# Kernel tuning notes

Measured on AMD Instinct MI355X. Metric: run time of the kernel, lower is better.

Reference implementation:

```python
import jax, jax.numpy as jnp
import numpy as np

B, S, D = 4, 2048, 1024
H, DK = 16, 64
NUM_BUCKETS = 32
MAX_DISTANCE = 128
EPS = 1e-6


def _relative_position_bucket(q_len, kv_len):
    # causal (bidirectional=False) T5 bucketization
    ctx = jnp.arange(q_len, dtype=jnp.int32)[:, None]
    mem = jnp.arange(kv_len, dtype=jnp.int32)[None, :]
    rp = mem - ctx                       # [q, kv]
    rp = -jnp.minimum(rp, 0)             # nonnegative distances to the past
    max_exact = NUM_BUCKETS // 2
    is_small = rp < max_exact
    rp_safe = jnp.maximum(rp, 1).astype(jnp.float32)
    large = max_exact + (
        jnp.log(rp_safe / max_exact) / np.log(MAX_DISTANCE / max_exact) * (NUM_BUCKETS - max_exact)
    ).astype(jnp.int32)
    large = jnp.minimum(large, NUM_BUCKETS - 1)
    return jnp.where(is_small, rp, large)  # [q, kv] int32 in [0, NUM_BUCKETS)


def setup_inputs() -> dict:
    key = jax.random.key(0)
    k1, k2, k3, k4 = jax.random.split(key, 4)
    hidden_states = jax.random.normal(k1, (B, S, D), dtype=jnp.float32)
    sequence_mask = jnp.ones((B, S), dtype=bool)
    rms_w = jnp.ones((D,), dtype=jnp.float32)
    W_qkv = jax.random.normal(k2, (D, 3 * H * DK), dtype=jnp.float32) * (D ** -0.5)
    W_o = jax.random.normal(k3, (H * DK, D), dtype=jnp.float32) * ((H * DK) ** -0.5)
    rel_bias = jax.random.normal(k4, (NUM_BUCKETS, H), dtype=jnp.float32)
    return {"hidden_states": hidden_states, "sequence_mask": sequence_mask,
            "rms_w": rms_w, "W_qkv": W_qkv, "W_o": W_o, "rel_bias": rel_bias}


def reference(hidden_states, sequence_mask, rms_w, W_qkv, W_o, rel_bias):
    # RMSNorm
    var = jnp.mean(hidden_states * hidden_states, axis=-1, keepdims=True)
    normed = hidden_states * jax.lax.rsqrt(var + EPS) * rms_w

    # QKV projection -> [B, S, 3, H, DK] -> [B, H, S, DK] each
    qkv = (normed @ W_qkv).reshape(B, S, 3, H, DK)
    q = jnp.transpose(qkv[:, :, 0], (0, 2, 1, 3))
    k = jnp.transpose(qkv[:, :, 1], (0, 2, 1, 3))
    v = jnp.transpose(qkv[:, :, 2], (0, 2, 1, 3))

    # relative position bias: gather [S,S,H] -> [1,H,S,S]
    bucket = _relative_position_bucket(S, S)
    pos_bias = jnp.transpose(rel_bias[bucket], (2, 0, 1))[None]

    # scores (note: T5 does NOT scale by 1/sqrt(dk))
    scores = jnp.einsum("bhqd,bhkd->bhqk", q, k) + pos_bias

    # causal mask combined with sequence mask (True = attend)
    causal = jnp.tril(jnp.ones((S, S), dtype=bool))
    mask = causal[None, None] & sequence_mask[:, None, None, :]
    scores = jnp.where(mask, scores, jnp.finfo(scores.dtype).min)

    attn = jax.nn.softmax(scores.astype(jnp.float32), axis=-1).astype(scores.dtype)
    # dropout p=0 / eval mode -> identity
    ctx = jnp.einsum("bhqk,bhkd->bhqd", attn, v)          # [B,H,S,DK]
    ctx = jnp.transpose(ctx, (0, 2, 1, 3)).reshape(B, S, H * DK)
    out = hidden_states + ctx @ W_o                        # residual
    return out
```

## Files before the change

kernel.cpp:

```cpp
#include <hip/hip_runtime.h>
#include <math.h>


typedef unsigned short ushort_t;
typedef __attribute__((ext_vector_type(8))) short bfrag;
typedef __attribute__((ext_vector_type(4))) float ffrag;

#define MFMA16(a, b, c) __builtin_amdgcn_mfma_f32_16x16x32_bf16((a), (b), (c), 0, 0, 0)
#define LOG2E 1.4426950408889634f

__device__ __forceinline__ void load_lds16(const ushort_t* g, ushort_t* l) {
  __builtin_amdgcn_global_load_lds(
      (const __attribute__((address_space(1))) unsigned int*)g,
      (__attribute__((address_space(3))) unsigned int*)l, 16, 0, 0);
}

__device__ __forceinline__ ushort_t f2bf(float f) {
  union { float f; unsigned u; } x; x.f = f;
  unsigned r = x.u + 0x7FFFu + ((x.u >> 16) & 1u);
  return (ushort_t)(r >> 16);
}
__device__ __forceinline__ float bf2f(ushort_t u) {
  union { unsigned u; float f; } x; x.u = ((unsigned)u) << 16; return x.f;
}
__device__ __forceinline__ unsigned cvtpk(float lo, float hi) {
  unsigned r;
  asm("v_cvt_pk_bf16_f32 %0, %1, %2" : "=v"(r) : "v"(lo), "v"(hi));
  return r;
}
__device__ __forceinline__ float exp2fast(float x) {
  return __builtin_amdgcn_exp2f(x);
}

__global__ __launch_bounds__(256) void norm_cvt_kernel(
    const float* __restrict__ hidden, const float* __restrict__ rms_w,
    ushort_t* __restrict__ normed) {
  const int w = threadIdx.x >> 6, lane = threadIdx.x & 63;
  const int row = blockIdx.x * 4 + w;
  const float* p = hidden + (size_t)row * 1024;
  float4 v[4];
  float s = 0.f;
#pragma unroll
  for (int i = 0; i < 4; ++i) {
    v[i] = *(const float4*)(p + (lane + i * 64) * 4);
    s += v[i].x * v[i].x + v[i].y * v[i].y + v[i].z * v[i].z + v[i].w * v[i].w;
  }
#pragma unroll
  for (int off = 1; off < 64; off <<= 1) s += __shfl_xor(s, off, 64);
  const float scale = rsqrtf(s * (1.0f / 1024.0f) + 1e-6f);
#pragma unroll
  for (int i = 0; i < 4; ++i) {
    const int c0 = (lane + i * 64) * 4;
    float4 wv = *(const float4*)(rms_w + c0);
    ushort4 u;
    u.x = f2bf(v[i].x * scale * wv.x);
    u.y = f2bf(v[i].y * scale * wv.y);
    u.z = f2bf(v[i].z * scale * wv.z);
    u.w = f2bf(v[i].w * scale * wv.w);
    *(ushort4*)(normed + (size_t)row * 1024 + c0) = u;
  }
}

__global__ __launch_bounds__(256) void transpose_cvt_kernel(
    const float* __restrict__ in, ushort_t* __restrict__ out, int R, int C) {
  __shared__ float tile[32][33];
  const int r0 = blockIdx.y * 32, c0 = blockIdx.x * 32;
  const int tr = threadIdx.x >> 5, tc = threadIdx.x & 31;
#pragma unroll
  for (int i = 0; i < 32; i += 8)
    tile[tr + i][tc] = in[(size_t)(r0 + tr + i) * C + c0 + tc];
  __syncthreads();
#pragma unroll
  for (int i = 0; i < 32; i += 8)
    out[(size_t)(c0 + tr + i) * R + r0 + tc] = f2bf(tile[tc][tr + i]);
}

__global__ __launch_bounds__(256) void qkv_mfma_kernel(
    const ushort_t* __restrict__ A, const ushort_t* __restrict__ Bt,
    ushort_t* __restrict__ qbf, ushort_t* __restrict__ kbf,
    ushort_t* __restrict__ vtbf) {
  __shared__ ushort_t At[128 * 32];
  __shared__ ushort_t Bs[128 * 32];
  const int tid = threadIdx.x, w = tid >> 6, lane = tid & 63;
  const int quad = lane >> 4, ln = lane & 15;
  const int wr = w >> 1, wc = w & 1;
  const int id = blockIdx.x;
  const int xcd = id & 7, t = id >> 3;
  const int by = xcd * 8 + t / 24, bx = t % 24;
  const int m0 = by * 128, n0 = bx * 128;
  const int srow = lane >> 2, scol = (lane & 3) * 8;

  ffrag acc[4][4];
#pragma unroll
  for (int i = 0; i < 4; ++i)
#pragma unroll
    for (int j = 0; j < 4; ++j) acc[i][j] = (ffrag)0.f;

  for (int kb = 0; kb < 1024; kb += 32) {
#pragma unroll
    for (int p = 0; p < 2; ++p) {
      load_lds16(A + (size_t)(m0 + (w * 2 + p) * 16 + srow) * 1024 + kb + scol,
                 At + (w * 2 + p) * 512);
      load_lds16(Bt + (size_t)(n0 + (w * 2 + p) * 16 + srow) * 1024 + kb + scol,
                 Bs + (w * 2 + p) * 512);
    }
    __syncthreads();
    bfrag a[4], b[4];
#pragma unroll
    for (int mi = 0; mi < 4; ++mi)
      a[mi] = *(const bfrag*)(At + (wr * 64 + mi * 16 + ln) * 32 + quad * 8);
#pragma unroll
    for (int ni = 0; ni < 4; ++ni)
      b[ni] = *(const bfrag*)(Bs + (wc * 64 + ni * 16 + ln) * 32 + quad * 8);
#pragma unroll
    for (int mi = 0; mi < 4; ++mi)
#pragma unroll
      for (int ni = 0; ni < 4; ++ni)
        acc[mi][ni] = MFMA16(a[mi], b[ni], acc[mi][ni]);
    __syncthreads();
  }

  const int b_idx = m0 >> 11;
  const int cbase = n0 + wc * 64 + ln;
#pragma unroll
  for (int mi = 0; mi < 4; ++mi) {
    const int sbase = (m0 & 2047) + wr * 64 + mi * 16 + quad * 4;
#pragma unroll
    for (int ni = 0; ni < 4; ++ni) {
      const int c = cbase + ni * 16;
      const int three = c >> 10, rem = c & 1023;
      const int h = rem >> 6, dk = rem & 63;
      if (three == 2) {
        ushort4 u;
        u.x = f2bf(acc[mi][ni][0]); u.y = f2bf(acc[mi][ni][1]);
        u.z = f2bf(acc[mi][ni][2]); u.w = f2bf(acc[mi][ni][3]);
        *(ushort4*)(vtbf + ((size_t)(b_idx * 16 + h) * 64 + dk) * 2048 + sbase) = u;
      } else {
        const float sc = (three == 0) ? 1.0f : LOG2E;
        ushort_t* dst = (three == 0 ? qbf : kbf) +
                        ((size_t)(b_idx * 16 + h) * 2048 + sbase) * 64 + dk;
        dst[0]   = f2bf(acc[mi][ni][0] * sc);
        dst[64]  = f2bf(acc[mi][ni][1] * sc);
        dst[128] = f2bf(acc[mi][ni][2] * sc);
        dst[192] = f2bf(acc[mi][ni][3] * sc);
      }
    }
  }
}

__global__ __launch_bounds__(512, 6) void attn_mfma_kernel(
    const ushort_t* __restrict__ qbf, const ushort_t* __restrict__ kbf,
    const ushort_t* __restrict__ vtbf, const float* __restrict__ rel_bias,
    ushort_t* __restrict__ ctx) {
  __shared__ ushort_t Kt[2][2][64][32];
  __shared__ ushort_t Vt[2][2][64][32];
  __shared__ ushort_t Pt[128][64];
  __shared__ ushort_t bias_t[2048];

  const int tid = threadIdx.x, w = tid >> 6, lane = tid & 63;
  const int quad = lane >> 4, ln = lane & 15;
  const int id = blockIdx.x;
  const int bh = id & 63;
  const int qb = 15 - (id >> 6);
  const int h = bh & 15;
  const int nt = 2 * qb + 2;
  const int q0w = qb * 128 + w * 16;

  for (int dist = tid; dist < 2048; dist += 512) {
    int bucket;
    if (dist < 16) bucket = dist;
    else {
      bucket = 16 + (int)(logf((float)dist * (1.0f / 16.0f)) * (16.0f / logf(8.0f)));
      if (bucket > 31) bucket = 31;
    }
    bias_t[dist] = f2bf(rel_bias[bucket * 16 + h] * LOG2E);
  }
  const float c31 = bf2f(f2bf(rel_bias[31 * 16 + h] * LOG2E));
  __syncthreads();

  const size_t khead = (size_t)bh * 2048 * 64;
  const int skf = tid >> 8;
  const int srow = (tid >> 2) & 63;
  const int ssw = ((tid & 3) ^ ((srow >> 1) & 3)) * 8;
  const int rsw = ((ln >> 1) & 3) * 8;
  const int psw = (ln & 7) * 8;

  bfrag aq[2];
#pragma unroll
  for (int kf = 0; kf < 2; ++kf)
    aq[kf] = *(const bfrag*)(qbf + ((size_t)bh * 2048 + q0w + ln) * 64 +
                             kf * 32 + quad * 8);

  bfrag ones;
#pragma unroll
  for (int i = 0; i < 8; ++i) ones[i] = (short)0x3F80;

  ffrag o[4], l_acc;
#pragma unroll
  for (int nd = 0; nd < 4; ++nd) o[nd] = (ffrag)0.f;
  l_acc = (ffrag)0.f;
  float m_run = -3.0e38f;

  load_lds16(kbf + khead + (size_t)srow * 64 + skf * 32 + ssw,
             &Kt[0][0][0][0] + tid * 8);
  load_lds16(vtbf + khead + (size_t)srow * 2048 + 0 + skf * 32 + ssw,
             &Vt[0][0][0][0] + tid * 8);

  int cur = 0;
  for (int j = 0; j < nt; ++j) {
    const int key0 = j * 64;
    asm volatile("s_waitcnt vmcnt(0)" ::: "memory");
    __builtin_amdgcn_s_barrier();

    if (j + 1 < nt) {
      const int nk0 = key0 + 64;
      load_lds16(kbf + khead + (size_t)(nk0 + srow) * 64 + skf * 32 + ssw,
                 &Kt[cur ^ 1][0][0][0] + tid * 8);
      load_lds16(vtbf + khead + (size_t)srow * 2048 + nk0 + skf * 32 + ssw,
                 &Vt[cur ^ 1][0][0][0] + tid * 8);
    }

    if (key0 <= q0w + 15) {
      ffrag s[4];
#pragma unroll
      for (int mi = 0; mi < 4; ++mi) s[mi] = (ffrag)0.f;
      __builtin_amdgcn_s_setprio(1);
#pragma unroll
      for (int kf = 0; kf < 2; ++kf)
#pragma unroll
        for (int mi = 0; mi < 4; ++mi) {
          bfrag ak = *(const bfrag*)&Kt[cur][kf][mi * 16 + ln][(quad * 8) ^ rsw];
          s[mi] = MFMA16(ak, aq[kf], s[mi]);
        }
      __builtin_amdgcn_s_setprio(0);

      const bool diagT = (key0 + 63 > q0w);
      const bool fastT = (key0 + 176 <= q0w);
      float sbias = 0.f;
      if (fastT) {
        sbias = c31;
      } else if (diagT) {
        const int q = q0w + ln;
#pragma unroll
        for (int mi = 0; mi < 4; ++mi) {
          const int keyb = key0 + mi * 16 + quad * 4;
#pragma unroll
          for (int r = 0; r < 4; ++r) {
            const int dist = q - (keyb + r);
            const int db = dist < 0 ? 0 : dist;
            s[mi][r] = (dist < 0) ? -3.0e38f : (s[mi][r] + bf2f(bias_t[db]));
          }
        }
      } else {
        const int q = q0w + ln;
#pragma unroll
        for (int mi = 0; mi < 4; ++mi) {
          const int keyb = key0 + mi * 16 + quad * 4;
#pragma unroll
          for (int r = 0; r < 4; ++r)
            s[mi][r] += bf2f(bias_t[q - (keyb + r)]);
        }
      }

      float m0_ = fmaxf(fmaxf(s[0][0], s[0][1]), fmaxf(s[0][2], s[0][3]));
      float m1_ = fmaxf(fmaxf(s[1][0], s[1][1]), fmaxf(s[1][2], s[1][3]));
      float m2_ = fmaxf(fmaxf(s[2][0], s[2][1]), fmaxf(s[2][2], s[2][3]));
      float m3_ = fmaxf(fmaxf(s[3][0], s[3][1]), fmaxf(s[3][2], s[3][3]));
      float mx = fmaxf(fmaxf(m0_, m1_), fmaxf(m2_, m3_));
      mx = fmaxf(mx, __shfl_xor(mx, 16, 64));
      mx = fmaxf(mx, __shfl_xor(mx, 32, 64));
      const float mxe = mx + sbias;

      if (!__all(mxe <= m_run + 8.0f)) {
        const float mnew = fmaxf(m_run, mxe);
        const float alpha = exp2fast(m_run - mnew);
        m_run = mnew;
#pragma unroll
        for (int r = 0; r < 4; ++r) {
          const float af = __shfl(alpha, quad * 4 + r, 64);
#pragma unroll
          for (int nd = 0; nd < 4; ++nd) o[nd][r] *= af;
          l_acc[r] *= af;
        }
      }
      const float sh = m_run - sbias;
#pragma unroll
      for (int mi = 0; mi < 4; ++mi)
#pragma unroll
        for (int r = 0; r < 4; ++r)
          s[mi][r] = exp2fast(s[mi][r] - sh);

      {
        ushort_t* prow = &Pt[w * 16 + ln][0];
#pragma unroll
        for (int mi = 0; mi < 4; ++mi) {
          uint2 pk;
          pk.x = cvtpk(s[mi][0], s[mi][1]);
          pk.y = cvtpk(s[mi][2], s[mi][3]);
          *(uint2*)(prow + ((mi * 16 + quad * 4) ^ psw)) = pk;
        }
      }

      __builtin_amdgcn_s_setprio(1);
#pragma unroll
      for (int kf = 0; kf < 2; ++kf) {
        bfrag ap = *(const bfrag*)&Pt[w * 16 + ln][(kf * 32 + quad * 8) ^ psw];
        l_acc = MFMA16(ap, ones, l_acc);
#pragma unroll
        for (int nd = 0; nd < 4; ++nd) {
          bfrag bv = *(const bfrag*)&Vt[cur][kf][nd * 16 + ln][(quad * 8) ^ rsw];
          o[nd] = MFMA16(ap, bv, o[nd]);
        }
      }
      __builtin_amdgcn_s_setprio(0);
    }
    cur ^= 1;
  }

  ffrag inv;
#pragma unroll
  for (int r = 0; r < 4; ++r) inv[r] = 1.0f / l_acc[r];
  const int s0 = q0w + quad * 4;
#pragma unroll
  for (int nd = 0; nd < 4; ++nd)
#pragma unroll
    for (int r = 0; r < 4; ++r)
      ctx[((size_t)(bh >> 4) * 2048 + s0 + r) * 1024 + h * 64 + nd * 16 + ln] =
          f2bf(o[nd][r] * inv[r]);
}

__global__ __launch_bounds__(256) void out_mfma_kernel(
    const ushort_t* __restrict__ A, const ushort_t* __restrict__ Bt,
    const float* __restrict__ hidden, float* __restrict__ out) {
  __shared__ ushort_t At[128 * 32];
  __shared__ ushort_t Bs[128 * 32];
  const int tid = threadIdx.x, w = tid >> 6, lane = tid & 63;
  const int quad = lane >> 4, ln = lane & 15;
  const int wr = w >> 1, wc = w & 1;
  const int id = blockIdx.x;
  const int xcd = id & 7, t = id >> 3;
  const int by = xcd * 8 + (t >> 3), bx = t & 7;
  const int m0 = by * 128, n0 = bx * 128;
  const int srow = lane >> 2, scol = (lane & 3) * 8;

  ffrag acc[4][4];
#pragma unroll
  for (int i = 0; i < 4; ++i)
#pragma unroll
    for (int j = 0; j < 4; ++j) acc[i][j] = (ffrag)0.f;

  for (int kb = 0; kb < 1024; kb += 32) {
#pragma unroll
    for (int p = 0; p < 2; ++p) {
      load_lds16(A + (size_t)(m0 + (w * 2 + p) * 16 + srow) * 1024 + kb + scol,
                 At + (w * 2 + p) * 512);
      load_lds16(Bt + (size_t)(n0 + (w * 2 + p) * 16 + srow) * 1024 + kb + scol,
                 Bs + (w * 2 + p) * 512);
    }
    __syncthreads();
    bfrag a[4], b[4];
#pragma unroll
    for (int mi = 0; mi < 4; ++mi)
      a[mi] = *(const bfrag*)(At + (wr * 64 + mi * 16 + ln) * 32 + quad * 8);
#pragma unroll
    for (int ni = 0; ni < 4; ++ni)
      b[ni] = *(const bfrag*)(Bs + (wc * 64 + ni * 16 + ln) * 32 + quad * 8);
#pragma unroll
    for (int mi = 0; mi < 4; ++mi)
#pragma unroll
      for (int ni = 0; ni < 4; ++ni)
        acc[mi][ni] = MFMA16(a[mi], b[ni], acc[mi][ni]);
    __syncthreads();
  }
#pragma unroll
  for (int mi = 0; mi < 4; ++mi) {
    const int m = m0 + wr * 64 + mi * 16 + quad * 4;
#pragma unroll
    for (int ni = 0; ni < 4; ++ni) {
      const int c = n0 + wc * 64 + ni * 16 + ln;
#pragma unroll
      for (int r = 0; r < 4; ++r) {
        const size_t off = (size_t)(m + r) * 1024 + c;
        out[off] = acc[mi][ni][r] + hidden[off];
      }
    }
  }
}

extern "C" void kernel_launch(void* const* d_in, const int* in_sizes, int n_in,
                              void* d_out, int out_size, void* d_ws, size_t ws_size,
                              hipStream_t stream) {
  const size_t NORMED = (size_t)8192 * 1024;
  const size_t WQKVT  = (size_t)3072 * 1024;
  const size_t WOT    = (size_t)1024 * 1024;
  const size_t QKVE   = (size_t)64 * 2048 * 64;
  const size_t need = (NORMED + WQKVT + WOT + 3 * QKVE + NORMED) * 2;
  if (ws_size < need) return;

  const float* hidden   = (const float*)d_in[0];
  const float* rms_w    = (const float*)d_in[2];
  const float* Wqkv     = (const float*)d_in[3];
  const float* Wo       = (const float*)d_in[4];
  const float* rel_bias = (const float*)d_in[5];
  float* out = (float*)d_out;

  ushort_t* normed = (ushort_t*)d_ws;
  ushort_t* wqkvt  = normed + NORMED;
  ushort_t* wot    = wqkvt + WQKVT;
  ushort_t* qbf    = wot + WOT;
  ushort_t* kbf    = qbf + QKVE;
  ushort_t* vtbf   = kbf + QKVE;
  ushort_t* ctx    = vtbf + QKVE;

  norm_cvt_kernel<<<2048, 256, 0, stream>>>(hidden, rms_w, normed);
  transpose_cvt_kernel<<<dim3(96, 32), 256, 0, stream>>>(Wqkv, wqkvt, 1024, 3072);
  transpose_cvt_kernel<<<dim3(32, 32), 256, 0, stream>>>(Wo, wot, 1024, 1024);
  qkv_mfma_kernel<<<1536, 256, 0, stream>>>(normed, wqkvt, qbf, kbf, vtbf);
  attn_mfma_kernel<<<1024, 512, 0, stream>>>(qbf, kbf, vtbf, rel_bias, ctx);
  out_mfma_kernel<<<512, 256, 0, stream>>>(ctx, wot, hidden, out);
}
```

Before: 278.5 us.

## Restructure QKV GEMM into 256x256 tiles with double-buffered swizzled LDS pipeline

Rewrites the QKV projection GEMM to use 256x256 output tiles with 8 waves, a 64-wide K step, and double-buffered LDS filled by direct global-to-LDS loads. The LDS layout is XOR-swizzled to avoid bank conflicts. Loads for the next K stages are interleaved with four MFMA quadrants, using explicit waitcnt, barriers and setprio. This aims to raise data reuse per tile and hide global memory latency behind matrix math, at the cost of more LDS, more registers and fewer blocks (384 on the GPU).

```diff
diff --git a/kernel.cpp b/kernel.cpp
--- a/kernel.cpp
+++ b/kernel.cpp
@@ -75,74 +75,174 @@
     out[(size_t)(c0 + tr + i) * R + r0 + tc] = f2bf(tile[tc][tr + i]);
 }
 
-__global__ __launch_bounds__(256) void qkv_mfma_kernel(
+__global__ __launch_bounds__(512) void qkv_mfma_kernel(
     const ushort_t* __restrict__ A, const ushort_t* __restrict__ Bt,
     ushort_t* __restrict__ qbf, ushort_t* __restrict__ kbf,
     ushort_t* __restrict__ vtbf) {
-  __shared__ ushort_t At[128 * 32];
-  __shared__ ushort_t Bs[128 * 32];
-  const int tid = threadIdx.x, w = tid >> 6, lane = tid & 63;
+  __shared__ ushort_t As[2][256][64];
+  __shared__ ushort_t Bs[2][256][64];
+  const int tid = threadIdx.x, lane = tid & 63, w = tid >> 6;
   const int quad = lane >> 4, ln = lane & 15;
-  const int wr = w >> 1, wc = w & 1;
+  const int wr = w >> 2, wc = w & 3;
   const int id = blockIdx.x;
-  const int xcd = id & 7, t = id >> 3;
-  const int by = xcd * 8 + t / 24, bx = t % 24;
-  const int m0 = by * 128, n0 = bx * 128;
-  const int srow = lane >> 2, scol = (lane & 3) * 8;
-
-  ffrag acc[4][4];
-#pragma unroll
-  for (int i = 0; i < 4; ++i)
+  const int xcd = id & 7, t8 = id >> 3;
+  const int by = xcd * 4 + t8 / 12, bx = t8 % 12;
+  const int m0 = by * 256, n0 = bx * 256;
+  const int rswz = ln & 7;
+
+  auto stageA = [&](int t, int h) {
+    ushort_t* lb = &As[t & 1][h * 128][0];
+    const int gr0 = m0 + h * 128, gc0 = t * 64;
+#pragma unroll
+    for (int i = 0; i < 2; ++i) {
+      const int idx = i * 512 + tid;
+      const int r = idx >> 3, c = idx & 7;
+      load_lds16(A + (size_t)(gr0 + r) * 1024 + gc0 + ((c ^ (r & 7)) * 8),
+                 lb + idx * 8);
+    }
+  };
+  auto stageB = [&](int t, int h) {
+    ushort_t* lb = &Bs[t & 1][h * 128][0];
+    const int gr0 = n0 + h * 128, gc0 = t * 64;
+#pragma unroll
+    for (int i = 0; i < 2; ++i) {
+      const int idx = i * 512 + tid;
+      const int r = idx >> 3, c = idx & 7;
+      load_lds16(Bt + (size_t)(gr0 + r) * 1024 + gc0 + ((c ^ (r & 7)) * 8),
+                 lb + idx * 8);
+    }
+  };
+
+  ffrag acc[8][4];
+#pragma unroll
+  for (int i = 0; i < 8; ++i)
 #pragma unroll
     for (int j = 0; j < 4; ++j) acc[i][j] = (ffrag)0.f;
 
-  for (int kb = 0; kb < 1024; kb += 32) {
-#pragma unroll
-    for (int p = 0; p < 2; ++p) {
-      load_lds16(A + (size_t)(m0 + (w * 2 + p) * 16 + srow) * 1024 + kb + scol,
-                 At + (w * 2 + p) * 512);
-      load_lds16(Bt + (size_t)(n0 + (w * 2 + p) * 16 + srow) * 1024 + kb + scol,
-                 Bs + (w * 2 + p) * 512);
-    }
-    __syncthreads();
-    bfrag a[4], b[4];
+  stageA(0, 0); stageA(0, 1); stageB(0, 0); stageB(0, 1);
+  stageB(1, 0); stageB(1, 1);
+  asm volatile("s_waitcnt vmcnt(4)" ::: "memory");
+  __builtin_amdgcn_s_barrier();
+
+  for (int t = 0; t < 16; ++t) {
+    const ushort_t* Ab = &As[t & 1][0][0];
+    const ushort_t* Bb = &Bs[t & 1][0][0];
+    bfrag a[4][2], b[4][2];
+
+#pragma unroll
+    for (int mi = 0; mi < 4; ++mi) {
+      const int rA = wr * 128 + mi * 16 + ln;
+#pragma unroll
+      for (int ks = 0; ks < 2; ++ks)
+        a[mi][ks] = *(const bfrag*)(Ab + rA * 64 + (((ks * 4 + quad) ^ rswz) * 8));
+    }
+#pragma unroll
+    for (int ni = 0; ni < 2; ++ni) {
+      const int rB = wc * 64 + ni * 16 + ln;
+#pragma unroll
+      for (int ks = 0; ks < 2; ++ks)
+        b[ni][ks] = *(const bfrag*)(Bb + rB * 64 + (((ks * 4 + quad) ^ rswz) * 8));
+    }
+    if (t + 1 < 16) stageA(t + 1, 0);
+    __builtin_amdgcn_s_barrier();
+    asm volatile("s_waitcnt lgkmcnt(0)" ::: "memory");
+    __builtin_amdgcn_sched_barrier(0);
+    __builtin_amdgcn_s_setprio(1);
 #pragma unroll
     for (int mi = 0; mi < 4; ++mi)
-      a[mi] = *(const bfrag*)(At + (wr * 64 + mi * 16 + ln) * 32 + quad * 8);
-#pragma unroll
-    for (int ni = 0; ni < 4; ++ni)
-      b[ni] = *(const bfrag*)(Bs + (wc * 64 + ni * 16 + ln) * 32 + quad * 8);
+#pragma unroll
+      for (int ni = 0; ni < 2; ++ni)
+#pragma unroll
+        for (int ks = 0; ks < 2; ++ks)
+          acc[mi][ni] = MFMA16(a[mi][ks], b[ni][ks], acc[mi][ni]);
+    __builtin_amdgcn_s_setprio(0);
+    __builtin_amdgcn_s_barrier();
+
+#pragma unroll
+    for (int ni = 0; ni < 2; ++ni) {
+      const int rB = wc * 64 + (2 + ni) * 16 + ln;
+#pragma unroll
+      for (int ks = 0; ks < 2; ++ks)
+        b[2 + ni][ks] = *(const bfrag*)(Bb + rB * 64 + (((ks * 4 + quad) ^ rswz) * 8));
+    }
+    if (t + 1 < 16) stageA(t + 1, 1);
+    __builtin_amdgcn_s_barrier();
+    asm volatile("s_waitcnt lgkmcnt(0)" ::: "memory");
+    __builtin_amdgcn_sched_barrier(0);
+    __builtin_amdgcn_s_setprio(1);
 #pragma unroll
     for (int mi = 0; mi < 4; ++mi)
 #pragma unroll
-      for (int ni = 0; ni < 4; ++ni)
-        acc[mi][ni] = MFMA16(a[mi], b[ni], acc[mi][ni]);
-    __syncthreads();
+      for (int ni = 0; ni < 2; ++ni)
+#pragma unroll
+        for (int ks = 0; ks < 2; ++ks)
+          acc[mi][2 + ni] = MFMA16(a[mi][ks], b[2 + ni][ks], acc[mi][2 + ni]);
+    __builtin_amdgcn_s_setprio(0);
+    __builtin_amdgcn_s_barrier();
+
+#pragma unroll
+    for (int mi = 0; mi < 4; ++mi) {
+      const int rA = wr * 128 + (4 + mi) * 16 + ln;
+#pragma unroll
+      for (int ks = 0; ks < 2; ++ks)
+        a[mi][ks] = *(const bfrag*)(Ab + rA * 64 + (((ks * 4 + quad) ^ rswz) * 8));
+    }
+    if (t + 2 < 16) stageB(t + 2, 0);
+    __builtin_amdgcn_s_barrier();
+    asm volatile("s_waitcnt lgkmcnt(0)" ::: "memory");
+    __builtin_amdgcn_sched_barrier(0);
+    __builtin_amdgcn_s_setprio(1);
+#pragma unroll
+    for (int mi = 0; mi < 4; ++mi)
+#pragma unroll
+      for (int ni = 0; ni < 2; ++ni)
+#pragma unroll
+        for (int ks = 0; ks < 2; ++ks)
+          acc[4 + mi][ni] = MFMA16(a[mi][ks], b[ni][ks], acc[4 + mi][ni]);
+    __builtin_amdgcn_s_setprio(0);
+    __builtin_amdgcn_s_barrier();
+
+    if (t + 2 < 16) stageB(t + 2, 1);
+    __builtin_amdgcn_s_barrier();
+    __builtin_amdgcn_s_setprio(1);
+#pragma unroll
+    for (int mi = 0; mi < 4; ++mi)
+#pragma unroll
+      for (int ni = 0; ni < 2; ++ni)
+#pragma unroll
+        for (int ks = 0; ks < 2; ++ks)
+          acc[4 + mi][2 + ni] = MFMA16(a[mi][ks], b[2 + ni][ks], acc[4 + mi][2 + ni]);
+    __builtin_amdgcn_s_setprio(0);
+    if (t < 15) {
+      if (t + 2 < 16) asm volatile("s_waitcnt vmcnt(4)" ::: "memory");
+      else            asm volatile("s_waitcnt vmcnt(0)" ::: "memory");
+      __builtin_amdgcn_s_barrier();
+    }
   }
 
   const int b_idx = m0 >> 11;
   const int cbase = n0 + wc * 64 + ln;
 #pragma unroll
-  for (int mi = 0; mi < 4; ++mi) {
-    const int sbase = (m0 & 2047) + wr * 64 + mi * 16 + quad * 4;
-#pragma unroll
-    for (int ni = 0; ni < 4; ++ni) {
-      const int c = cbase + ni * 16;
+  for (int mf = 0; mf < 8; ++mf) {
+    const int sbase = (m0 & 2047) + wr * 128 + mf * 16 + quad * 4;
+#pragma unroll
+    for (int nf = 0; nf < 4; ++nf) {
+      const int c = cbase + nf * 16;
       const int three = c >> 10, rem = c & 1023;
       const int h = rem >> 6, dk = rem & 63;
       if (three == 2) {
         ushort4 u;
-        u.x = f2bf(acc[mi][ni][0]); u.y = f2bf(acc[mi][ni][1]);
-        u.z = f2bf(acc[mi][ni][2]); u.w = f2bf(acc[mi][ni][3]);
+        u.x = f2bf(acc[mf][nf][0]); u.y = f2bf(acc[mf][nf][1]);
+        u.z = f2bf(acc[mf][nf][2]); u.w = f2bf(acc[mf][nf][3]);
         *(ushort4*)(vtbf + ((size_t)(b_idx * 16 + h) * 64 + dk) * 2048 + sbase) = u;
       } else {
         const float sc = (three == 0) ? 1.0f : LOG2E;
         ushort_t* dst = (three == 0 ? qbf : kbf) +
                         ((size_t)(b_idx * 16 + h) * 2048 + sbase) * 64 + dk;
-        dst[0]   = f2bf(acc[mi][ni][0] * sc);
-        dst[64]  = f2bf(acc[mi][ni][1] * sc);
-        dst[128] = f2bf(acc[mi][ni][2] * sc);
-        dst[192] = f2bf(acc[mi][ni][3] * sc);
+        dst[0]   = f2bf(acc[mf][nf][0] * sc);
+        dst[64]  = f2bf(acc[mf][nf][1] * sc);
+        dst[128] = f2bf(acc[mf][nf][2] * sc);
+        dst[192] = f2bf(acc[mf][nf][3] * sc);
       }
     }
   }
@@ -415,7 +515,7 @@
   norm_cvt_kernel<<<2048, 256, 0, stream>>>(hidden, rms_w, normed);
   transpose_cvt_kernel<<<dim3(96, 32), 256, 0, stream>>>(Wqkv, wqkvt, 1024, 3072);
   transpose_cvt_kernel<<<dim3(32, 32), 256, 0, stream>>>(Wo, wot, 1024, 1024);
-  qkv_mfma_kernel<<<1536, 256, 0, stream>>>(normed, wqkvt, qbf, kbf, vtbf);
+  qkv_mfma_kernel<<<384, 512, 0, stream>>>(normed, wqkvt, qbf, kbf, vtbf);
   attn_mfma_kernel<<<1024, 512, 0, stream>>>(qbf, kbf, vtbf, rel_bias, ctx);
   out_mfma_kernel<<<512, 256, 0, stream>>>(ctx, wot, hidden, out);
 }
```

Result: no change. 274.0 us (-1.6%).

## Double-buffer GEMM K-loop with swizzled LDS tiles and defer softmax max shuffles

Applied to the files above, without the earlier changes.

Both projection GEMMs now stage 64-wide K tiles into double-buffered LDS with an XOR swizzle, prefetching the next tile while MFMAs run on the current one, and raise wave priority around the MFMA block. This halves the barrier count and overlaps global loads with compute, at the cost of four times the LDS per block (64 KB). The attention softmax also skips the cross-lane max shuffles unless a rescale is actually needed, removing per-tile shuffle latency. One risk is that the WAR on the buffer being prefetched relies on the end-of-iteration barrier.

```diff
diff --git a/kernel.cpp b/kernel.cpp
--- a/kernel.cpp
+++ b/kernel.cpp
@@ -75,20 +75,30 @@
     out[(size_t)(c0 + tr + i) * R + r0 + tc] = f2bf(tile[tc][tr + i]);
 }
 
-__global__ __launch_bounds__(256) void qkv_mfma_kernel(
+__global__ __launch_bounds__(256, 2) void qkv_mfma_kernel(
     const ushort_t* __restrict__ A, const ushort_t* __restrict__ Bt,
     ushort_t* __restrict__ qbf, ushort_t* __restrict__ kbf,
     ushort_t* __restrict__ vtbf) {
-  __shared__ ushort_t At[128 * 32];
-  __shared__ ushort_t Bs[128 * 32];
-  const int tid = threadIdx.x, w = tid >> 6, lane = tid & 63;
+  __shared__ ushort_t As[2][128][64];
+  __shared__ ushort_t Bs[2][128][64];
+  const int tid = threadIdx.x, lane = tid & 63, w = tid >> 6;
   const int quad = lane >> 4, ln = lane & 15;
   const int wr = w >> 1, wc = w & 1;
   const int id = blockIdx.x;
-  const int xcd = id & 7, t = id >> 3;
-  const int by = xcd * 8 + t / 24, bx = t % 24;
+  const int xcd = id & 7, t8 = id >> 3;
+  const int by = xcd * 8 + t8 / 24, bx = t8 % 24;
   const int m0 = by * 128, n0 = bx * 128;
-  const int srow = lane >> 2, scol = (lane & 3) * 8;
+  const int rswz = ln & 7;
+
+  auto stage = [&](const ushort_t* src, ushort_t* lds, int gr0, int gc0) {
+#pragma unroll
+    for (int i = 0; i < 4; ++i) {
+      const int idx = i * 256 + tid;
+      const int r = idx >> 3, c = idx & 7;
+      load_lds16(src + (size_t)(gr0 + r) * 1024 + gc0 + ((c ^ (r & 7)) * 8),
+                 lds + idx * 8);
+    }
+  };
 
   ffrag acc[4][4];
 #pragma unroll
@@ -96,28 +106,43 @@
 #pragma unroll
     for (int j = 0; j < 4; ++j) acc[i][j] = (ffrag)0.f;
 
-  for (int kb = 0; kb < 1024; kb += 32) {
-#pragma unroll
-    for (int p = 0; p < 2; ++p) {
-      load_lds16(A + (size_t)(m0 + (w * 2 + p) * 16 + srow) * 1024 + kb + scol,
-                 At + (w * 2 + p) * 512);
-      load_lds16(Bt + (size_t)(n0 + (w * 2 + p) * 16 + srow) * 1024 + kb + scol,
-                 Bs + (w * 2 + p) * 512);
-    }
-    __syncthreads();
-    bfrag a[4], b[4];
+  stage(A, &As[0][0][0], m0, 0);
+  stage(Bt, &Bs[0][0][0], n0, 0);
+  asm volatile("s_waitcnt vmcnt(0)" ::: "memory");
+  __builtin_amdgcn_s_barrier();
+
+  for (int t = 0; t < 16; ++t) {
+    const int cur = t & 1;
+    if (t + 1 < 16) {
+      stage(A, &As[cur ^ 1][0][0], m0, (t + 1) * 64);
+      stage(Bt, &Bs[cur ^ 1][0][0], n0, (t + 1) * 64);
+    }
+    bfrag a[4][2], b[4][2];
+#pragma unroll
+    for (int mi = 0; mi < 4; ++mi) {
+      const int rA = wr * 64 + mi * 16 + ln;
+#pragma unroll
+      for (int ks = 0; ks < 2; ++ks)
+        a[mi][ks] = *(const bfrag*)(&As[cur][rA][((ks * 4 + quad) ^ rswz) * 8]);
+    }
+#pragma unroll
+    for (int ni = 0; ni < 4; ++ni) {
+      const int rB = wc * 64 + ni * 16 + ln;
+#pragma unroll
+      for (int ks = 0; ks < 2; ++ks)
+        b[ni][ks] = *(const bfrag*)(&Bs[cur][rB][((ks * 4 + quad) ^ rswz) * 8]);
+    }
+    __builtin_amdgcn_s_setprio(1);
 #pragma unroll
     for (int mi = 0; mi < 4; ++mi)
-      a[mi] = *(const bfrag*)(At + (wr * 64 + mi * 16 + ln) * 32 + quad * 8);
-#pragma unroll
-    for (int ni = 0; ni < 4; ++ni)
-      b[ni] = *(const bfrag*)(Bs + (wc * 64 + ni * 16 + ln) * 32 + quad * 8);
-#pragma unroll
-    for (int mi = 0; mi < 4; ++mi)
 #pragma unroll
       for (int ni = 0; ni < 4; ++ni)
-        acc[mi][ni] = MFMA16(a[mi], b[ni], acc[mi][ni]);
-    __syncthreads();
+#pragma unroll
+        for (int ks = 0; ks < 2; ++ks)
+          acc[mi][ni] = MFMA16(a[mi][ks], b[ni][ks], acc[mi][ni]);
+    __builtin_amdgcn_s_setprio(0);
+    asm volatile("s_waitcnt vmcnt(0)" ::: "memory");
+    __builtin_amdgcn_s_barrier();
   }
 
   const int b_idx = m0 >> 11;
@@ -266,13 +291,13 @@
       float m1_ = fmaxf(fmaxf(s[1][0], s[1][1]), fmaxf(s[1][2], s[1][3]));
       float m2_ = fmaxf(fmaxf(s[2][0], s[2][1]), fmaxf(s[2][2], s[2][3]));
       float m3_ = fmaxf(fmaxf(s[3][0], s[3][1]), fmaxf(s[3][2], s[3][3]));
-      float mx = fmaxf(fmaxf(m0_, m1_), fmaxf(m2_, m3_));
-      mx = fmaxf(mx, __shfl_xor(mx, 16, 64));
-      mx = fmaxf(mx, __shfl_xor(mx, 32, 64));
-      const float mxe = mx + sbias;
-
-      if (!__all(mxe <= m_run + 8.0f)) {
-        const float mnew = fmaxf(m_run, mxe);
+      const float mxl = fmaxf(fmaxf(m0_, m1_), fmaxf(m2_, m3_)) + sbias;
+
+      if (!__all(mxl <= m_run + 8.0f)) {
+        float mx = mxl;
+        mx = fmaxf(mx, __shfl_xor(mx, 16, 64));
+        mx = fmaxf(mx, __shfl_xor(mx, 32, 64));
+        const float mnew = fmaxf(m_run, mx);
         const float alpha = exp2fast(m_run - mnew);
         m_run = mnew;
 #pragma unroll
@@ -329,19 +354,29 @@
           f2bf(o[nd][r] * inv[r]);
 }
 
-__global__ __launch_bounds__(256) void out_mfma_kernel(
+__global__ __launch_bounds__(256, 2) void out_mfma_kernel(
     const ushort_t* __restrict__ A, const ushort_t* __restrict__ Bt,
     const float* __restrict__ hidden, float* __restrict__ out) {
-  __shared__ ushort_t At[128 * 32];
-  __shared__ ushort_t Bs[128 * 32];
-  const int tid = threadIdx.x, w = tid >> 6, lane = tid & 63;
+  __shared__ ushort_t As[2][128][64];
+  __shared__ ushort_t Bs[2][128][64];
+  const int tid = threadIdx.x, lane = tid & 63, w = tid >> 6;
   const int quad = lane >> 4, ln = lane & 15;
   const int wr = w >> 1, wc = w & 1;
   const int id = blockIdx.x;
   const int xcd = id & 7, t = id >> 3;
   const int by = xcd * 8 + (t >> 3), bx = t & 7;
   const int m0 = by * 128, n0 = bx * 128;
-  const int srow = lane >> 2, scol = (lane & 3) * 8;
+  const int rswz = ln & 7;
+
+  auto stage = [&](const ushort_t* src, ushort_t* lds, int gr0, int gc0) {
+#pragma unroll
+    for (int i = 0; i < 4; ++i) {
+      const int idx = i * 256 + tid;
+      const int r = idx >> 3, c = idx & 7;
+      load_lds16(src + (size_t)(gr0 + r) * 1024 + gc0 + ((c ^ (r & 7)) * 8),
+                 lds + idx * 8);
+    }
+  };
 
   ffrag acc[4][4];
 #pragma unroll
@@ -349,29 +384,45 @@
 #pragma unroll
     for (int j = 0; j < 4; ++j) acc[i][j] = (ffrag)0.f;
 
-  for (int kb = 0; kb < 1024; kb += 32) {
-#pragma unroll
-    for (int p = 0; p < 2; ++p) {
-      load_lds16(A + (size_t)(m0 + (w * 2 + p) * 16 + srow) * 1024 + kb + scol,
-                 At + (w * 2 + p) * 512);
-      load_lds16(Bt + (size_t)(n0 + (w * 2 + p) * 16 + srow) * 1024 + kb + scol,
-                 Bs + (w * 2 + p) * 512);
-    }
-    __syncthreads();
-    bfrag a[4], b[4];
+  stage(A, &As[0][0][0], m0, 0);
+  stage(Bt, &Bs[0][0][0], n0, 0);
+  asm volatile("s_waitcnt vmcnt(0)" ::: "memory");
+  __builtin_amdgcn_s_barrier();
+
+  for (int t2 = 0; t2 < 16; ++t2) {
+    const int cur = t2 & 1;
+    if (t2 + 1 < 16) {
+      stage(A, &As[cur ^ 1][0][0], m0, (t2 + 1) * 64);
+      stage(Bt, &Bs[cur ^ 1][0][0], n0, (t2 + 1) * 64);
+    }
+    bfrag a[4][2], b[4][2];
+#pragma unroll
+    for (int mi = 0; mi < 4; ++mi) {
+      const int rA = wr * 64 + mi * 16 + ln;
+#pragma unroll
+      for (int ks = 0; ks < 2; ++ks)
+        a[mi][ks] = *(const bfrag*)(&As[cur][rA][((ks * 4 + quad) ^ rswz) * 8]);
+    }
+#pragma unroll
+    for (int ni = 0; ni < 4; ++ni) {
+      const int rB = wc * 64 + ni * 16 + ln;
+#pragma unroll
+      for (int ks = 0; ks < 2; ++ks)
+        b[ni][ks] = *(const bfrag*)(&Bs[cur][rB][((ks * 4 + quad) ^ rswz) * 8]);
+    }
+    __builtin_amdgcn_s_setprio(1);
 #pragma unroll
     for (int mi = 0; mi < 4; ++mi)
-      a[mi] = *(const bfrag*)(At + (wr * 64 + mi * 16 + ln) * 32 + quad * 8);
-#pragma unroll
-    for (int ni = 0; ni < 4; ++ni)
-      b[ni] = *(const bfrag*)(Bs + (wc * 64 + ni * 16 + ln) * 32 + quad * 8);
-#pragma unroll
-    for (int mi = 0; mi < 4; ++mi)
 #pragma unroll
       for (int ni = 0; ni < 4; ++ni)
-        acc[mi][ni] = MFMA16(a[mi], b[ni], acc[mi][ni]);
-    __syncthreads();
-  }
+#pragma unroll
+        for (int ks = 0; ks < 2; ++ks)
+          acc[mi][ni] = MFMA16(a[mi][ks], b[ni][ks], acc[mi][ni]);
+    __builtin_amdgcn_s_setprio(0);
+    asm volatile("s_waitcnt vmcnt(0)" ::: "memory");
+    __builtin_amdgcn_s_barrier();
+  }
+
 #pragma unroll
   for (int mi = 0; mi < 4; ++mi) {
     const int m = m0 + wr * 64 + mi * 16 + quad * 4;
```

After: 258.7 us. 1.08x faster.
